# Performance work log

Measured on AMD Instinct MI355X. Metric: run time of the kernel, lower is better.

Reference implementation:

```python
import jax, jax.numpy as jnp
import numpy as np


def setup_inputs() -> dict:
    key = jax.random.key(0)
    ks = jax.random.split(key, 5)
    B, D, U = 16384, 512, 512
    return {
        "inputs": jax.random.normal(ks[0], (B, D), dtype=jnp.float32),
        "h_prev": jax.random.normal(ks[1], (B, U), dtype=jnp.float32),
        "update_kernel": jax.random.normal(ks[2], (D + U, U), dtype=jnp.float32) * 0.03,
        "reset_kernel": jax.random.normal(ks[3], (D + U, U), dtype=jnp.float32) * 0.03,
        "hidden_kernel": jax.random.normal(ks[4], (D + U, U), dtype=jnp.float32) * 0.03,
        "update_bias": jnp.zeros((U,), dtype=jnp.float32),
        "reset_bias": jnp.zeros((U,), dtype=jnp.float32),
        "hidden_bias": jnp.zeros((U,), dtype=jnp.float32),
    }


def reference(inputs, h_prev, update_kernel, reset_kernel, hidden_kernel,
              update_bias, reset_bias, hidden_bias):
    # fused_input: [B, D+U]
    fused = jnp.concatenate([inputs, h_prev], axis=-1)
    zg = jax.nn.sigmoid(fused @ update_kernel + update_bias)   # update gate [B,U]
    rg = jax.nn.sigmoid(fused @ reset_kernel + reset_bias)     # reset gate  [B,U]
    h_tilde = jnp.tanh(
        jnp.concatenate([inputs, rg * h_prev], axis=-1) @ hidden_kernel + hidden_bias
    )
    ht = (1.0 - zg) * h_prev + zg * h_tilde
    return ht
```

## Files before the change

### kernel.cpp

```cpp
#include <hip/hip_runtime.h>
#include <hip/hip_bf16.h>
#include <math.h>

typedef __attribute__((ext_vector_type(4))) float f32x4;
typedef __attribute__((ext_vector_type(8))) float f32x8;
typedef __bf16 bf16x8 __attribute__((ext_vector_type(8)));
typedef unsigned short u16;
typedef u16 u16x8 __attribute__((ext_vector_type(8)));
typedef void __attribute__((address_space(1))) * as1p;
typedef void __attribute__((address_space(3))) * as3p;

__device__ __forceinline__ unsigned short f2bf(float f) {
    union { float f; unsigned int u; } v; v.f = f;
    unsigned int u = v.u;
    u += 0x7fffu + ((u >> 16) & 1u);
    return (unsigned short)(u >> 16);
}

__device__ __forceinline__ float bf2f(unsigned short b) {
    union { unsigned int u; float f; } v;
    v.u = ((unsigned int)b) << 16;
    return v.f;
}

__device__ __forceinline__ float fast_tanh(float v) {
    float vc = fminf(fmaxf(v, -15.f), 15.f);
    float e = __expf(2.f * vc);
    return (e - 1.f) / (e + 1.f);
}

__global__ void prep_k(const float* __restrict__ x, const float* __restrict__ h,
                       const float* __restrict__ wz, const float* __restrict__ wrr,
                       const float* __restrict__ wh,
                       u16* __restrict__ xb, u16* __restrict__ hb,
                       u16* __restrict__ wzt, u16* __restrict__ wrt, u16* __restrict__ wht) {
    __shared__ float t[32][33];
    int bid = blockIdx.x;
    int tid = threadIdx.x;
    if (bid < 2048) {
        const int n4 = 16384 * 512 / 4;
        int i = bid * 256 + tid;
        const int stride = 2048 * 256;
        const float4* x4 = (const float4*)x;
        const float4* h4 = (const float4*)h;
        ushort4* xb4 = (ushort4*)xb;
        ushort4* hb4 = (ushort4*)hb;
        for (; i < n4; i += stride) {
            float4 v = x4[i];
            xb4[i] = make_ushort4(f2bf(v.x), f2bf(v.y), f2bf(v.z), f2bf(v.w));
            float4 w = h4[i];
            hb4[i] = make_ushort4(f2bf(w.x), f2bf(w.y), f2bf(w.z), f2bf(w.w));
        }
    } else {
        int b = bid - 2048;
        int z = b >> 9;
        int rem = b & 511;
        const float* src = (z == 0) ? wz : (z == 1) ? wrr : wh;
        u16* dst = (z == 0) ? wzt : (z == 1) ? wrt : wht;
        int n0 = (rem & 15) * 32;
        int k0 = (rem >> 4) * 32;
        int tx = tid & 31, ty = tid >> 5;
#pragma unroll
        for (int i = 0; i < 4; ++i)
            t[ty + i * 8][tx] = src[(size_t)(k0 + ty + i * 8) * 512 + n0 + tx];
        __syncthreads();
#pragma unroll
        for (int i = 0; i < 4; ++i)
            dst[(size_t)(n0 + ty + i * 8) * 1024 + k0 + tx] = f2bf(t[tx][ty + i * 8]);
    }
}

__device__ __forceinline__ void stage_sw(const u16* g, int gstride, u16* lds, int tid) {
#pragma unroll
    for (int i = 0; i < 4; ++i) {
        int ob = i * 4096 + ((tid >> 6) << 10);
        int o = ob + ((tid & 63) << 4);
        int row = o >> 7;
        int cb = (o & 127) ^ ((row & 7) << 4);
        const u16* gp = g + (size_t)row * gstride + (cb >> 1);
        __builtin_amdgcn_global_load_lds((as1p)(void*)gp, (as3p)(void*)(lds + (ob >> 1)), 16, 0, 0);
    }
}

__device__ __forceinline__ bf16x8 ld_frag(const u16* region, int r, int kb) {
    int byte = (r << 7) + (kb ^ ((r & 7) << 4));
    return *(const bf16x8*)((const char*)region + byte);
}

__device__ __forceinline__ void compute_tile(const u16* LA, const u16* LB,
                                             int wr, int wc, int l, f32x4 (&acc)[4][4]) {
    int fr = l & 15;
    int kbb = (l >> 4) << 4;
#pragma unroll
    for (int q = 0; q < 2; ++q) {
        bf16x8 a[4], b[4];
#pragma unroll
        for (int m = 0; m < 4; ++m)
            a[m] = ld_frag(LA, wr * 64 + m * 16 + fr, q * 64 + kbb);
#pragma unroll
        for (int n = 0; n < 4; ++n)
            b[n] = ld_frag(LB, wc * 64 + n * 16 + fr, q * 64 + kbb);
#pragma unroll
        for (int m = 0; m < 4; ++m)
#pragma unroll
            for (int n = 0; n < 4; ++n)
                acc[m][n] = __builtin_amdgcn_mfma_f32_16x16x32_bf16(a[m], b[n], acc[m][n], 0, 0, 0);
    }
}

template<typename AF, typename BF>
__device__ __forceinline__ void kloop(AF ga, BF gb, u16* lds, int tid,
                                      int wr, int wc, int l, f32x4 (&acc)[4][4]) {
    stage_sw(ga(0), 512, lds, tid);
    stage_sw(gb(0), 1024, lds + 8192, tid);
    __syncthreads();
#pragma unroll
    for (int i = 0; i < 15; ++i) {
        u16* nxt = lds + ((i + 1) & 1) * 16384;
        const u16* cur = lds + (i & 1) * 16384;
        stage_sw(ga(i + 1), 512, nxt, tid);
        stage_sw(gb(i + 1), 1024, nxt + 8192, tid);
        compute_tile(cur, cur + 8192, wr, wc, l, acc);
        __syncthreads();
    }
    compute_tile(lds + 16384, lds + 16384 + 8192, wr, wc, l, acc);
}

__device__ __forceinline__ void scatter_acc(float* tf, const f32x4 (&acc)[4][4],
                                            int wr, int wc, int l) {
    int colb = wc * 64;
    int rowb = wr * 64 + ((l >> 4) << 2);
#pragma unroll
    for (int n = 0; n < 4; ++n) {
        int col = colb + n * 16 + (l & 15);
#pragma unroll
        for (int m = 0; m < 4; ++m) {
            int row0 = rowb + m * 16;
#pragma unroll
            for (int r = 0; r < 4; ++r)
                tf[(row0 + r) * 128 + col] = acc[m][n][r];
        }
    }
}

__global__ __launch_bounds__(256) void gr_k(
    const u16* __restrict__ Xb, const u16* __restrict__ Hb, const u16* __restrict__ Wt,
    const float* __restrict__ rb_, u16* __restrict__ rgh) {
    __shared__ u16 lds[2 * 16384];
    int tid = threadIdx.x;
    int l = tid & 63, w = tid >> 6;
    int wr = w >> 1, wc = w & 1;
    int swz = (blockIdx.x & 7) * 64 + (blockIdx.x >> 3);
    int mb = swz >> 2, nb = swz & 3;
    int m0 = mb * 128, n0 = nb * 128;
    f32x4 acc[4][4];
#pragma unroll
    for (int m = 0; m < 4; ++m)
#pragma unroll
        for (int n = 0; n < 4; ++n) acc[m][n] = (f32x4){0.f, 0.f, 0.f, 0.f};

    auto ga = [&](int t) -> const u16* {
        return (t < 8) ? (Xb + (size_t)m0 * 512 + t * 64)
                       : (Hb + (size_t)m0 * 512 + (t - 8) * 64);
    };
    auto gb = [&](int t) -> const u16* { return Wt + (size_t)n0 * 1024 + t * 64; };
    kloop(ga, gb, lds, tid, wr, wc, l, acc);

    __syncthreads();
    float* tf = (float*)lds;
    scatter_acc(tf, acc, wr, wc, l);
    __syncthreads();
#pragma unroll
    for (int i = 0; i < 8; ++i) {
        int chunk = i * 256 + tid;
        int row = chunk >> 4;
        int c8 = (chunk & 15) << 3;
        const float* src = &tf[row * 128 + c8];
        int gcol = n0 + c8;
        size_t gbase = (size_t)(m0 + row) * 512 + gcol;
        u16x8 h8 = *(const u16x8*)&Hb[gbase];
        u16x8 o;
#pragma unroll
        for (int j = 0; j < 8; ++j) {
            float v = src[j] + rb_[gcol + j];
            float s = 1.f / (1.f + __expf(-v));
            o[j] = f2bf(s * bf2f(h8[j]));
        }
        *(u16x8*)&rgh[gbase] = o;
    }
}

__device__ __forceinline__ void stage32(const u16* g, int gstride, u16* region, int tid) {
#pragma unroll
    for (int i = 0; i < 2; ++i) {
        int ob = i * 4096 + ((tid >> 6) << 10);
        int o = ob + ((tid & 63) << 4);
        int row = o >> 6;
        int cb = (o & 63) ^ ((row & 6) << 3);
        const u16* gp = g + (size_t)row * gstride + (cb >> 1);
        __builtin_amdgcn_global_load_lds((as1p)(void*)gp, (as3p)(void*)(region + (ob >> 1)), 16, 0, 0);
    }
}

__device__ __forceinline__ bf16x8 ld32(const u16* region, int r, int kb) {
    int byte = (r << 6) + (kb ^ ((r & 6) << 3));
    return *(const bf16x8*)((const char*)region + byte);
}

__global__ __launch_bounds__(256, 2) void ghz_k(
    const u16* __restrict__ Xb, const u16* __restrict__ Hb, const u16* __restrict__ rgh,
    const u16* __restrict__ Wht, const u16* __restrict__ Wzt,
    const float* __restrict__ ub, const float* __restrict__ hb,
    float* __restrict__ out) {
    __shared__ u16 lds[2 * 16384];
    int tid = threadIdx.x;
    int l = tid & 63, w = tid >> 6;
    int wr = w >> 1, wc = w & 1;
    int swz = (blockIdx.x & 7) * 64 + (blockIdx.x >> 3);
    int mb = swz >> 2, nb = swz & 3;
    int m0 = mb * 128, n0 = nb * 128;

    f32x4 acc_h[4][4], acc_z[4][4];
#pragma unroll
    for (int m = 0; m < 4; ++m)
#pragma unroll
        for (int n = 0; n < 4; ++n) {
            acc_h[m][n] = (f32x4){0.f, 0.f, 0.f, 0.f};
            acc_z[m][n] = (f32x4){0.f, 0.f, 0.f, 0.f};
        }

    auto ah = [&](int t) -> const u16* {
        return (t < 16) ? (Xb + (size_t)m0 * 512 + t * 32)
                        : (rgh + (size_t)m0 * 512 + (t - 16) * 32);
    };
    auto az = [&](int t) -> const u16* {
        return Hb + (size_t)m0 * 512 + (t - 16) * 32;
    };
    auto bhp = [&](int t) -> const u16* { return Wht + (size_t)n0 * 1024 + t * 32; };
    auto bzp = [&](int t) -> const u16* { return Wzt + (size_t)n0 * 1024 + t * 32; };

    const int fr = l & 15;
    const int kbb = (l >> 4) << 4;

    stage32(ah(0), 512, lds, tid);
    stage32(bhp(0), 1024, lds + 8192, tid);
    stage32(bzp(0), 1024, lds + 12288, tid);
    __syncthreads();

#pragma unroll
    for (int i = 0; i < 32; ++i) {
        const u16* cur = lds + (i & 1) * 16384;
        if (i < 31) {
            u16* nxt = lds + ((i + 1) & 1) * 16384;
            stage32(ah(i + 1), 512, nxt, tid);
            if (i + 1 >= 16) stage32(az(i + 1), 512, nxt + 4096, tid);
            stage32(bhp(i + 1), 1024, nxt + 8192, tid);
            stage32(bzp(i + 1), 1024, nxt + 12288, tid);
        }
        const u16* Ahr = cur;
        const u16* Azr = (i < 16) ? cur : (cur + 4096);
        const u16* Bhr = cur + 8192;
        const u16* Bzr = cur + 12288;
        bf16x8 a[4], azf[4], bh4[4], bz4[4];
#pragma unroll
        for (int m = 0; m < 4; ++m) {
            a[m]   = ld32(Ahr, wr * 64 + m * 16 + fr, kbb);
            azf[m] = ld32(Azr, wr * 64 + m * 16 + fr, kbb);
        }
#pragma unroll
        for (int n = 0; n < 4; ++n) {
            bh4[n] = ld32(Bhr, wc * 64 + n * 16 + fr, kbb);
            bz4[n] = ld32(Bzr, wc * 64 + n * 16 + fr, kbb);
        }
#pragma unroll
        for (int m = 0; m < 4; ++m)
#pragma unroll
            for (int n = 0; n < 4; ++n) {
                acc_h[m][n] = __builtin_amdgcn_mfma_f32_16x16x32_bf16(a[m], bh4[n], acc_h[m][n], 0, 0, 0);
                acc_z[m][n] = __builtin_amdgcn_mfma_f32_16x16x32_bf16(azf[m], bz4[n], acc_z[m][n], 0, 0, 0);
            }
        __syncthreads();
    }

    float* tf = (float*)lds;
    scatter_acc(tf, acc_z, wr, wc, l);
    __syncthreads();
    u16x8 zreg[8];
#pragma unroll
    for (int i = 0; i < 8; ++i) {
        int chunk = i * 256 + tid;
        int row = chunk >> 4;
        int c8 = (chunk & 15) << 3;
        f32x8 vz = *(const f32x8*)&tf[row * 128 + c8];
        f32x8 ubv = *(const f32x8*)&ub[n0 + c8];
#pragma unroll
        for (int j = 0; j < 8; ++j) {
            float s = 1.f / (1.f + __expf(-(vz[j] + ubv[j])));
            zreg[i][j] = f2bf(s);
        }
    }
    __syncthreads();
    scatter_acc(tf, acc_h, wr, wc, l);
    __syncthreads();
#pragma unroll
    for (int i = 0; i < 8; ++i) {
        int chunk = i * 256 + tid;
        int row = chunk >> 4;
        int c8 = (chunk & 15) << 3;
        int gcol = n0 + c8;
        size_t gbase = (size_t)(m0 + row) * 512 + gcol;
        f32x8 vh = *(const f32x8*)&tf[row * 128 + c8];
        f32x8 hbv = *(const f32x8*)&hb[gcol];
        u16x8 h8 = *(const u16x8*)&Hb[gbase];
        f32x8 o;
#pragma unroll
        for (int j = 0; j < 8; ++j) {
            float t = fast_tanh(vh[j] + hbv[j]);
            float h0 = bf2f(h8[j]);
            float z = bf2f(zreg[i][j]);
            o[j] = h0 + z * (t - h0);
        }
        *(f32x8*)&out[gbase] = o;
    }
}

extern "C" void kernel_launch(void* const* d_in, const int* in_sizes, int n_in,
                              void* d_out, int out_size, void* d_ws, size_t ws_size,
                              hipStream_t stream) {
    const float* x  = (const float*)d_in[0];
    const float* h  = (const float*)d_in[1];
    const float* wz = (const float*)d_in[2];
    const float* wr = (const float*)d_in[3];
    const float* wh = (const float*)d_in[4];
    const float* ub = (const float*)d_in[5];
    const float* rb = (const float*)d_in[6];
    const float* hb = (const float*)d_in[7];
    float* out = (float*)d_out;

    const int B = 16384;
    char* ws = (char*)d_ws;
    size_t off = 0;
    u16* Xb  = (u16*)(ws + off); off += (size_t)B * 512 * 2;
    u16* Hb  = (u16*)(ws + off); off += (size_t)B * 512 * 2;
    u16* Wzt = (u16*)(ws + off); off += (size_t)512 * 1024 * 2;
    u16* Wrt = (u16*)(ws + off); off += (size_t)512 * 1024 * 2;
    u16* Wht = (u16*)(ws + off); off += (size_t)512 * 1024 * 2;
    u16* rgh = (u16*)(ws + off); off += (size_t)B * 512 * 2;

    prep_k<<<2048 + 1536, 256, 0, stream>>>(x, h, wz, wr, wh, Xb, Hb, Wzt, Wrt, Wht);

    gr_k<<<512, 256, 0, stream>>>(Xb, Hb, Wrt, rb, rgh);
    ghz_k<<<512, 256, 0, stream>>>(Xb, Hb, rgh, Wht, Wzt, ub, hb, out);
}
```

Before: 98.24 us.

## Halve GEMM N-tile to 64 and shrink LDS for higher occupancy

```diff
diff --git a/kernel.cpp b/kernel.cpp
--- a/kernel.cpp
+++ b/kernel.cpp
@@ -70,127 +70,7 @@
     }
 }
 
-__device__ __forceinline__ void stage_sw(const u16* g, int gstride, u16* lds, int tid) {
-#pragma unroll
-    for (int i = 0; i < 4; ++i) {
-        int ob = i * 4096 + ((tid >> 6) << 10);
-        int o = ob + ((tid & 63) << 4);
-        int row = o >> 7;
-        int cb = (o & 127) ^ ((row & 7) << 4);
-        const u16* gp = g + (size_t)row * gstride + (cb >> 1);
-        __builtin_amdgcn_global_load_lds((as1p)(void*)gp, (as3p)(void*)(lds + (ob >> 1)), 16, 0, 0);
-    }
-}
-
-__device__ __forceinline__ bf16x8 ld_frag(const u16* region, int r, int kb) {
-    int byte = (r << 7) + (kb ^ ((r & 7) << 4));
-    return *(const bf16x8*)((const char*)region + byte);
-}
-
-__device__ __forceinline__ void compute_tile(const u16* LA, const u16* LB,
-                                             int wr, int wc, int l, f32x4 (&acc)[4][4]) {
-    int fr = l & 15;
-    int kbb = (l >> 4) << 4;
-#pragma unroll
-    for (int q = 0; q < 2; ++q) {
-        bf16x8 a[4], b[4];
-#pragma unroll
-        for (int m = 0; m < 4; ++m)
-            a[m] = ld_frag(LA, wr * 64 + m * 16 + fr, q * 64 + kbb);
-#pragma unroll
-        for (int n = 0; n < 4; ++n)
-            b[n] = ld_frag(LB, wc * 64 + n * 16 + fr, q * 64 + kbb);
-#pragma unroll
-        for (int m = 0; m < 4; ++m)
-#pragma unroll
-            for (int n = 0; n < 4; ++n)
-                acc[m][n] = __builtin_amdgcn_mfma_f32_16x16x32_bf16(a[m], b[n], acc[m][n], 0, 0, 0);
-    }
-}
-
-template<typename AF, typename BF>
-__device__ __forceinline__ void kloop(AF ga, BF gb, u16* lds, int tid,
-                                      int wr, int wc, int l, f32x4 (&acc)[4][4]) {
-    stage_sw(ga(0), 512, lds, tid);
-    stage_sw(gb(0), 1024, lds + 8192, tid);
-    __syncthreads();
-#pragma unroll
-    for (int i = 0; i < 15; ++i) {
-        u16* nxt = lds + ((i + 1) & 1) * 16384;
-        const u16* cur = lds + (i & 1) * 16384;
-        stage_sw(ga(i + 1), 512, nxt, tid);
-        stage_sw(gb(i + 1), 1024, nxt + 8192, tid);
-        compute_tile(cur, cur + 8192, wr, wc, l, acc);
-        __syncthreads();
-    }
-    compute_tile(lds + 16384, lds + 16384 + 8192, wr, wc, l, acc);
-}
-
-__device__ __forceinline__ void scatter_acc(float* tf, const f32x4 (&acc)[4][4],
-                                            int wr, int wc, int l) {
-    int colb = wc * 64;
-    int rowb = wr * 64 + ((l >> 4) << 2);
-#pragma unroll
-    for (int n = 0; n < 4; ++n) {
-        int col = colb + n * 16 + (l & 15);
-#pragma unroll
-        for (int m = 0; m < 4; ++m) {
-            int row0 = rowb + m * 16;
-#pragma unroll
-            for (int r = 0; r < 4; ++r)
-                tf[(row0 + r) * 128 + col] = acc[m][n][r];
-        }
-    }
-}
-
-__global__ __launch_bounds__(256) void gr_k(
-    const u16* __restrict__ Xb, const u16* __restrict__ Hb, const u16* __restrict__ Wt,
-    const float* __restrict__ rb_, u16* __restrict__ rgh) {
-    __shared__ u16 lds[2 * 16384];
-    int tid = threadIdx.x;
-    int l = tid & 63, w = tid >> 6;
-    int wr = w >> 1, wc = w & 1;
-    int swz = (blockIdx.x & 7) * 64 + (blockIdx.x >> 3);
-    int mb = swz >> 2, nb = swz & 3;
-    int m0 = mb * 128, n0 = nb * 128;
-    f32x4 acc[4][4];
-#pragma unroll
-    for (int m = 0; m < 4; ++m)
-#pragma unroll
-        for (int n = 0; n < 4; ++n) acc[m][n] = (f32x4){0.f, 0.f, 0.f, 0.f};
-
-    auto ga = [&](int t) -> const u16* {
-        return (t < 8) ? (Xb + (size_t)m0 * 512 + t * 64)
-                       : (Hb + (size_t)m0 * 512 + (t - 8) * 64);
-    };
-    auto gb = [&](int t) -> const u16* { return Wt + (size_t)n0 * 1024 + t * 64; };
-    kloop(ga, gb, lds, tid, wr, wc, l, acc);
-
-    __syncthreads();
-    float* tf = (float*)lds;
-    scatter_acc(tf, acc, wr, wc, l);
-    __syncthreads();
-#pragma unroll
-    for (int i = 0; i < 8; ++i) {
-        int chunk = i * 256 + tid;
-        int row = chunk >> 4;
-        int c8 = (chunk & 15) << 3;
-        const float* src = &tf[row * 128 + c8];
-        int gcol = n0 + c8;
-        size_t gbase = (size_t)(m0 + row) * 512 + gcol;
-        u16x8 h8 = *(const u16x8*)&Hb[gbase];
-        u16x8 o;
-#pragma unroll
-        for (int j = 0; j < 8; ++j) {
-            float v = src[j] + rb_[gcol + j];
-            float s = 1.f / (1.f + __expf(-v));
-            o[j] = f2bf(s * bf2f(h8[j]));
-        }
-        *(u16x8*)&rgh[gbase] = o;
-    }
-}
-
-__device__ __forceinline__ void stage32(const u16* g, int gstride, u16* region, int tid) {
+__device__ __forceinline__ void stageA32(const u16* g, int gstride, u16* region, int tid) {
 #pragma unroll
     for (int i = 0; i < 2; ++i) {
         int ob = i * 4096 + ((tid >> 6) << 10);
@@ -202,32 +82,153 @@
     }
 }
 
+__device__ __forceinline__ void stageB32(const u16* g, int gstride, u16* region, int tid) {
+    int ob = (tid >> 6) << 10;
+    int o = ob + ((tid & 63) << 4);
+    int row = o >> 6;
+    int cb = (o & 63) ^ ((row & 6) << 3);
+    const u16* gp = g + (size_t)row * gstride + (cb >> 1);
+    __builtin_amdgcn_global_load_lds((as1p)(void*)gp, (as3p)(void*)(region + (ob >> 1)), 16, 0, 0);
+}
+
 __device__ __forceinline__ bf16x8 ld32(const u16* region, int r, int kb) {
     int byte = (r << 6) + (kb ^ ((r & 6) << 3));
     return *(const bf16x8*)((const char*)region + byte);
 }
 
-__global__ __launch_bounds__(256, 2) void ghz_k(
+__device__ __forceinline__ void scatter64(float* tf, const f32x4 (&acc)[4][2],
+                                          int wr, int wc, int l) {
+    int colb = wc * 32;
+    int rowb = wr * 64 + ((l >> 4) << 2);
+#pragma unroll
+    for (int n = 0; n < 2; ++n) {
+        int col = colb + n * 16 + (l & 15);
+#pragma unroll
+        for (int m = 0; m < 4; ++m) {
+            int row0 = rowb + m * 16;
+#pragma unroll
+            for (int r = 0; r < 4; ++r)
+                tf[(row0 + r) * 64 + col] = acc[m][n][r];
+        }
+    }
+}
+
+__global__ __launch_bounds__(256, 4) void gr_k(
+    const u16* __restrict__ Xb, const u16* __restrict__ Hb, const u16* __restrict__ Wt,
+    const float* __restrict__ rb_, u16* __restrict__ rgh) {
+    __shared__ u16 lds[16384];
+    int tid = threadIdx.x;
+    int l = tid & 63, w = tid >> 6;
+    int wr = w >> 1, wc = w & 1;
+    int bid = blockIdx.x;
+    int swz = (bid & 7) * 128 + (bid >> 3);
+    int mb = swz >> 3, nbv = swz & 7;
+    int m0 = mb * 128, n0 = nbv * 64;
+    f32x4 acc[4][2];
+#pragma unroll
+    for (int m = 0; m < 4; ++m)
+#pragma unroll
+        for (int n = 0; n < 2; ++n) acc[m][n] = (f32x4){0.f, 0.f, 0.f, 0.f};
+
+    const int fr = l & 15;
+    const int kbb = (l >> 4) << 4;
+
+    auto ga = [&](int t) -> const u16* {
+        return (t < 16) ? (Xb + (size_t)m0 * 512 + t * 32)
+                        : (Hb + (size_t)m0 * 512 + (t - 16) * 32);
+    };
+    auto gb = [&](int t) -> const u16* { return Wt + (size_t)n0 * 1024 + t * 32; };
+
+    stageA32(ga(0), 512, lds, tid);
+    stageB32(gb(0), 1024, lds + 4096, tid);
+    __syncthreads();
+#pragma unroll
+    for (int i = 0; i < 31; ++i) {
+        u16* nxt = lds + ((i + 1) & 1) * 6144;
+        const u16* cur = lds + (i & 1) * 6144;
+        stageA32(ga(i + 1), 512, nxt, tid);
+        stageB32(gb(i + 1), 1024, nxt + 4096, tid);
+        {
+            bf16x8 a[4], b[2];
+#pragma unroll
+            for (int m = 0; m < 4; ++m)
+                a[m] = ld32(cur, wr * 64 + m * 16 + fr, kbb);
+#pragma unroll
+            for (int n = 0; n < 2; ++n)
+                b[n] = ld32(cur + 4096, wc * 32 + n * 16 + fr, kbb);
+#pragma unroll
+            for (int m = 0; m < 4; ++m)
+#pragma unroll
+                for (int n = 0; n < 2; ++n)
+                    acc[m][n] = __builtin_amdgcn_mfma_f32_16x16x32_bf16(a[m], b[n], acc[m][n], 0, 0, 0);
+        }
+        __syncthreads();
+    }
+    {
+        const u16* cur = lds + (31 & 1) * 6144;
+        bf16x8 a[4], b[2];
+#pragma unroll
+        for (int m = 0; m < 4; ++m)
+            a[m] = ld32(cur, wr * 64 + m * 16 + fr, kbb);
+#pragma unroll
+        for (int n = 0; n < 2; ++n)
+            b[n] = ld32(cur + 4096, wc * 32 + n * 16 + fr, kbb);
+#pragma unroll
+        for (int m = 0; m < 4; ++m)
+#pragma unroll
+            for (int n = 0; n < 2; ++n)
+                acc[m][n] = __builtin_amdgcn_mfma_f32_16x16x32_bf16(a[m], b[n], acc[m][n], 0, 0, 0);
+    }
+
+    __syncthreads();
+    float* tf = (float*)lds;
+    scatter64(tf, acc, wr, wc, l);
+    __syncthreads();
+#pragma unroll
+    for (int it = 0; it < 4; ++it) {
+        int chunk = it * 256 + tid;
+        int row = chunk >> 3;
+        int c8 = (chunk & 7) << 3;
+        const float* src = &tf[row * 64 + c8];
+        int gcol = n0 + c8;
+        size_t gbase = (size_t)(m0 + row) * 512 + gcol;
+        u16x8 h8 = *(const u16x8*)&Hb[gbase];
+        u16x8 o;
+#pragma unroll
+        for (int j = 0; j < 8; ++j) {
+            float v = src[j] + rb_[gcol + j];
+            float s = 1.f / (1.f + __expf(-v));
+            o[j] = f2bf(s * bf2f(h8[j]));
+        }
+        *(u16x8*)&rgh[gbase] = o;
+    }
+}
+
+__global__ __launch_bounds__(256, 3) void ghz_k(
     const u16* __restrict__ Xb, const u16* __restrict__ Hb, const u16* __restrict__ rgh,
     const u16* __restrict__ Wht, const u16* __restrict__ Wzt,
     const float* __restrict__ ub, const float* __restrict__ hb,
     float* __restrict__ out) {
-    __shared__ u16 lds[2 * 16384];
+    __shared__ u16 lds[24576];
     int tid = threadIdx.x;
     int l = tid & 63, w = tid >> 6;
     int wr = w >> 1, wc = w & 1;
-    int swz = (blockIdx.x & 7) * 64 + (blockIdx.x >> 3);
-    int mb = swz >> 2, nb = swz & 3;
-    int m0 = mb * 128, n0 = nb * 128;
-
-    f32x4 acc_h[4][4], acc_z[4][4];
+    int bid = blockIdx.x;
+    int swz = (bid & 7) * 128 + (bid >> 3);
+    int mb = swz >> 3, nbv = swz & 7;
+    int m0 = mb * 128, n0 = nbv * 64;
+
+    f32x4 acc_h[4][2], acc_z[4][2];
 #pragma unroll
     for (int m = 0; m < 4; ++m)
 #pragma unroll
-        for (int n = 0; n < 4; ++n) {
+        for (int n = 0; n < 2; ++n) {
             acc_h[m][n] = (f32x4){0.f, 0.f, 0.f, 0.f};
             acc_z[m][n] = (f32x4){0.f, 0.f, 0.f, 0.f};
         }
+
+    const int fr = l & 15;
+    const int kbb = (l >> 4) << 4;
 
     auto ah = [&](int t) -> const u16* {
         return (t < 16) ? (Xb + (size_t)m0 * 512 + t * 32)
@@ -239,77 +240,74 @@
     auto bhp = [&](int t) -> const u16* { return Wht + (size_t)n0 * 1024 + t * 32; };
     auto bzp = [&](int t) -> const u16* { return Wzt + (size_t)n0 * 1024 + t * 32; };
 
-    const int fr = l & 15;
-    const int kbb = (l >> 4) << 4;
-
-    stage32(ah(0), 512, lds, tid);
-    stage32(bhp(0), 1024, lds + 8192, tid);
-    stage32(bzp(0), 1024, lds + 12288, tid);
+    stageA32(ah(0), 512, lds, tid);
+    stageB32(bhp(0), 1024, lds + 8192, tid);
+    stageB32(bzp(0), 1024, lds + 10240, tid);
     __syncthreads();
 
 #pragma unroll
     for (int i = 0; i < 32; ++i) {
-        const u16* cur = lds + (i & 1) * 16384;
+        const u16* cur = lds + (i & 1) * 12288;
         if (i < 31) {
-            u16* nxt = lds + ((i + 1) & 1) * 16384;
-            stage32(ah(i + 1), 512, nxt, tid);
-            if (i + 1 >= 16) stage32(az(i + 1), 512, nxt + 4096, tid);
-            stage32(bhp(i + 1), 1024, nxt + 8192, tid);
-            stage32(bzp(i + 1), 1024, nxt + 12288, tid);
+            u16* nxt = lds + ((i + 1) & 1) * 12288;
+            stageA32(ah(i + 1), 512, nxt, tid);
+            if (i + 1 >= 16) stageA32(az(i + 1), 512, nxt + 4096, tid);
+            stageB32(bhp(i + 1), 1024, nxt + 8192, tid);
+            stageB32(bzp(i + 1), 1024, nxt + 10240, tid);
         }
         const u16* Ahr = cur;
         const u16* Azr = (i < 16) ? cur : (cur + 4096);
         const u16* Bhr = cur + 8192;
-        const u16* Bzr = cur + 12288;
-        bf16x8 a[4], azf[4], bh4[4], bz4[4];
+        const u16* Bzr = cur + 10240;
+        bf16x8 a[4], azf[4], bh2[2], bz2[2];
 #pragma unroll
         for (int m = 0; m < 4; ++m) {
             a[m]   = ld32(Ahr, wr * 64 + m * 16 + fr, kbb);
             azf[m] = ld32(Azr, wr * 64 + m * 16 + fr, kbb);
         }
 #pragma unroll
-        for (int n = 0; n < 4; ++n) {
-            bh4[n] = ld32(Bhr, wc * 64 + n * 16 + fr, kbb);
-            bz4[n] = ld32(Bzr, wc * 64 + n * 16 + fr, kbb);
+        for (int n = 0; n < 2; ++n) {
+            bh2[n] = ld32(Bhr, wc * 32 + n * 16 + fr, kbb);
+            bz2[n] = ld32(Bzr, wc * 32 + n * 16 + fr, kbb);
         }
 #pragma unroll
         for (int m = 0; m < 4; ++m)
 #pragma unroll
-            for (int n = 0; n < 4; ++n) {
-                acc_h[m][n] = __builtin_amdgcn_mfma_f32_16x16x32_bf16(a[m], bh4[n], acc_h[m][n], 0, 0, 0);
-                acc_z[m][n] = __builtin_amdgcn_mfma_f32_16x16x32_bf16(azf[m], bz4[n], acc_z[m][n], 0, 0, 0);
+            for (int n = 0; n < 2; ++n) {
+                acc_h[m][n] = __builtin_amdgcn_mfma_f32_16x16x32_bf16(a[m], bh2[n], acc_h[m][n], 0, 0, 0);
+                acc_z[m][n] = __builtin_amdgcn_mfma_f32_16x16x32_bf16(azf[m], bz2[n], acc_z[m][n], 0, 0, 0);
             }
         __syncthreads();
     }
 
     float* tf = (float*)lds;
-    scatter_acc(tf, acc_z, wr, wc, l);
-    __syncthreads();
-    u16x8 zreg[8];
-#pragma unroll
-    for (int i = 0; i < 8; ++i) {
-        int chunk = i * 256 + tid;
-        int row = chunk >> 4;
-        int c8 = (chunk & 15) << 3;
-        f32x8 vz = *(const f32x8*)&tf[row * 128 + c8];
+    scatter64(tf, acc_z, wr, wc, l);
+    __syncthreads();
+    u16x8 zreg[4];
+#pragma unroll
+    for (int it = 0; it < 4; ++it) {
+        int chunk = it * 256 + tid;
+        int row = chunk >> 3;
+        int c8 = (chunk & 7) << 3;
+        f32x8 vz = *(const f32x8*)&tf[row * 64 + c8];
         f32x8 ubv = *(const f32x8*)&ub[n0 + c8];
 #pragma unroll
         for (int j = 0; j < 8; ++j) {
             float s = 1.f / (1.f + __expf(-(vz[j] + ubv[j])));
-            zreg[i][j] = f2bf(s);
-        }
-    }
-    __syncthreads();
-    scatter_acc(tf, acc_h, wr, wc, l);
-    __syncthreads();
-#pragma unroll
-    for (int i = 0; i < 8; ++i) {
-        int chunk = i * 256 + tid;
-        int row = chunk >> 4;
-        int c8 = (chunk & 15) << 3;
+            zreg[it][j] = f2bf(s);
+        }
+    }
+    __syncthreads();
+    scatter64(tf, acc_h, wr, wc, l);
+    __syncthreads();
+#pragma unroll
+    for (int it = 0; it < 4; ++it) {
+        int chunk = it * 256 + tid;
+        int row = chunk >> 3;
+        int c8 = (chunk & 7) << 3;
         int gcol = n0 + c8;
         size_t gbase = (size_t)(m0 + row) * 512 + gcol;
-        f32x8 vh = *(const f32x8*)&tf[row * 128 + c8];
+        f32x8 vh = *(const f32x8*)&tf[row * 64 + c8];
         f32x8 hbv = *(const f32x8*)&hb[gcol];
         u16x8 h8 = *(const u16x8*)&Hb[gbase];
         f32x8 o;
@@ -317,7 +315,7 @@
         for (int j = 0; j < 8; ++j) {
             float t = fast_tanh(vh[j] + hbv[j]);
             float h0 = bf2f(h8[j]);
-            float z = bf2f(zreg[i][j]);
+            float z = bf2f(zreg[it][j]);
             o[j] = h0 + z * (t - h0);
         }
         *(f32x8*)&out[gbase] = o;
@@ -349,6 +347,6 @@
 
     prep_k<<<2048 + 1536, 256, 0, stream>>>(x, h, wz, wr, wh, Xb, Hb, Wzt, Wrt, Wht);
 
-    gr_k<<<512, 256, 0, stream>>>(Xb, Hb, Wrt, rb, rgh);
-    ghz_k<<<512, 256, 0, stream>>>(Xb, Hb, rgh, Wht, Wzt, ub, hb, out);
-}
+    gr_k<<<1024, 256, 0, stream>>>(Xb, Hb, Wrt, rb, rgh);
+    ghz_k<<<1024, 256, 0, stream>>>(Xb, Hb, rgh, Wht, Wzt, ub, hb, out);
+}
```

New measurement: 106.3 us. 8.2% more time.

## Halve ghz_k N-tile to 64 columns and double grid for occupancy

Applied to the files above, without the earlier changes.

```diff
diff --git a/kernel.cpp b/kernel.cpp
--- a/kernel.cpp
+++ b/kernel.cpp
@@ -190,7 +190,7 @@
     }
 }
 
-__device__ __forceinline__ void stage32(const u16* g, int gstride, u16* region, int tid) {
+__device__ __forceinline__ void stageA32(const u16* g, int gstride, u16* region, int tid) {
 #pragma unroll
     for (int i = 0; i < 2; ++i) {
         int ob = i * 4096 + ((tid >> 6) << 10);
@@ -202,32 +202,62 @@
     }
 }
 
+__device__ __forceinline__ void stageB32(const u16* g, int gstride, u16* region, int tid) {
+    int ob = (tid >> 6) << 10;
+    int o = ob + ((tid & 63) << 4);
+    int row = o >> 6;
+    int cb = (o & 63) ^ ((row & 6) << 3);
+    const u16* gp = g + (size_t)row * gstride + (cb >> 1);
+    __builtin_amdgcn_global_load_lds((as1p)(void*)gp, (as3p)(void*)(region + (ob >> 1)), 16, 0, 0);
+}
+
 __device__ __forceinline__ bf16x8 ld32(const u16* region, int r, int kb) {
     int byte = (r << 6) + (kb ^ ((r & 6) << 3));
     return *(const bf16x8*)((const char*)region + byte);
 }
 
-__global__ __launch_bounds__(256, 2) void ghz_k(
+__device__ __forceinline__ void scatter64(float* tf, const f32x4 (&acc)[4][2],
+                                          int wr, int wc, int l) {
+    int colb = wc * 32;
+    int rowb = wr * 64 + ((l >> 4) << 2);
+#pragma unroll
+    for (int n = 0; n < 2; ++n) {
+        int col = colb + n * 16 + (l & 15);
+#pragma unroll
+        for (int m = 0; m < 4; ++m) {
+            int row0 = rowb + m * 16;
+#pragma unroll
+            for (int r = 0; r < 4; ++r)
+                tf[(row0 + r) * 64 + col] = acc[m][n][r];
+        }
+    }
+}
+
+__global__ __launch_bounds__(256, 3) void ghz_k(
     const u16* __restrict__ Xb, const u16* __restrict__ Hb, const u16* __restrict__ rgh,
     const u16* __restrict__ Wht, const u16* __restrict__ Wzt,
     const float* __restrict__ ub, const float* __restrict__ hb,
     float* __restrict__ out) {
-    __shared__ u16 lds[2 * 16384];
+    __shared__ u16 lds[24576];
     int tid = threadIdx.x;
     int l = tid & 63, w = tid >> 6;
     int wr = w >> 1, wc = w & 1;
-    int swz = (blockIdx.x & 7) * 64 + (blockIdx.x >> 3);
-    int mb = swz >> 2, nb = swz & 3;
-    int m0 = mb * 128, n0 = nb * 128;
-
-    f32x4 acc_h[4][4], acc_z[4][4];
+    int bid = blockIdx.x;
+    int swz = (bid & 7) * 128 + (bid >> 3);
+    int mb = swz >> 3, nbv = swz & 7;
+    int m0 = mb * 128, n0 = nbv * 64;
+
+    f32x4 acc_h[4][2], acc_z[4][2];
 #pragma unroll
     for (int m = 0; m < 4; ++m)
 #pragma unroll
-        for (int n = 0; n < 4; ++n) {
+        for (int n = 0; n < 2; ++n) {
             acc_h[m][n] = (f32x4){0.f, 0.f, 0.f, 0.f};
             acc_z[m][n] = (f32x4){0.f, 0.f, 0.f, 0.f};
         }
+
+    const int fr = l & 15;
+    const int kbb = (l >> 4) << 4;
 
     auto ah = [&](int t) -> const u16* {
         return (t < 16) ? (Xb + (size_t)m0 * 512 + t * 32)
@@ -239,77 +269,74 @@
     auto bhp = [&](int t) -> const u16* { return Wht + (size_t)n0 * 1024 + t * 32; };
     auto bzp = [&](int t) -> const u16* { return Wzt + (size_t)n0 * 1024 + t * 32; };
 
-    const int fr = l & 15;
-    const int kbb = (l >> 4) << 4;
-
-    stage32(ah(0), 512, lds, tid);
-    stage32(bhp(0), 1024, lds + 8192, tid);
-    stage32(bzp(0), 1024, lds + 12288, tid);
+    stageA32(ah(0), 512, lds, tid);
+    stageB32(bhp(0), 1024, lds + 8192, tid);
+    stageB32(bzp(0), 1024, lds + 10240, tid);
     __syncthreads();
 
 #pragma unroll
     for (int i = 0; i < 32; ++i) {
-        const u16* cur = lds + (i & 1) * 16384;
+        const u16* cur = lds + (i & 1) * 12288;
         if (i < 31) {
-            u16* nxt = lds + ((i + 1) & 1) * 16384;
-            stage32(ah(i + 1), 512, nxt, tid);
-            if (i + 1 >= 16) stage32(az(i + 1), 512, nxt + 4096, tid);
-            stage32(bhp(i + 1), 1024, nxt + 8192, tid);
-            stage32(bzp(i + 1), 1024, nxt + 12288, tid);
+            u16* nxt = lds + ((i + 1) & 1) * 12288;
+            stageA32(ah(i + 1), 512, nxt, tid);
+            if (i + 1 >= 16) stageA32(az(i + 1), 512, nxt + 4096, tid);
+            stageB32(bhp(i + 1), 1024, nxt + 8192, tid);
+            stageB32(bzp(i + 1), 1024, nxt + 10240, tid);
         }
         const u16* Ahr = cur;
         const u16* Azr = (i < 16) ? cur : (cur + 4096);
         const u16* Bhr = cur + 8192;
-        const u16* Bzr = cur + 12288;
-        bf16x8 a[4], azf[4], bh4[4], bz4[4];
+        const u16* Bzr = cur + 10240;
+        bf16x8 a[4], azf[4], bh2[2], bz2[2];
 #pragma unroll
         for (int m = 0; m < 4; ++m) {
             a[m]   = ld32(Ahr, wr * 64 + m * 16 + fr, kbb);
             azf[m] = ld32(Azr, wr * 64 + m * 16 + fr, kbb);
         }
 #pragma unroll
-        for (int n = 0; n < 4; ++n) {
-            bh4[n] = ld32(Bhr, wc * 64 + n * 16 + fr, kbb);
-            bz4[n] = ld32(Bzr, wc * 64 + n * 16 + fr, kbb);
+        for (int n = 0; n < 2; ++n) {
+            bh2[n] = ld32(Bhr, wc * 32 + n * 16 + fr, kbb);
+            bz2[n] = ld32(Bzr, wc * 32 + n * 16 + fr, kbb);
         }
 #pragma unroll
         for (int m = 0; m < 4; ++m)
 #pragma unroll
-            for (int n = 0; n < 4; ++n) {
-                acc_h[m][n] = __builtin_amdgcn_mfma_f32_16x16x32_bf16(a[m], bh4[n], acc_h[m][n], 0, 0, 0);
-                acc_z[m][n] = __builtin_amdgcn_mfma_f32_16x16x32_bf16(azf[m], bz4[n], acc_z[m][n], 0, 0, 0);
+            for (int n = 0; n < 2; ++n) {
+                acc_h[m][n] = __builtin_amdgcn_mfma_f32_16x16x32_bf16(a[m], bh2[n], acc_h[m][n], 0, 0, 0);
+                acc_z[m][n] = __builtin_amdgcn_mfma_f32_16x16x32_bf16(azf[m], bz2[n], acc_z[m][n], 0, 0, 0);
             }
         __syncthreads();
     }
 
     float* tf = (float*)lds;
-    scatter_acc(tf, acc_z, wr, wc, l);
-    __syncthreads();
-    u16x8 zreg[8];
-#pragma unroll
-    for (int i = 0; i < 8; ++i) {
-        int chunk = i * 256 + tid;
-        int row = chunk >> 4;
-        int c8 = (chunk & 15) << 3;
-        f32x8 vz = *(const f32x8*)&tf[row * 128 + c8];
+    scatter64(tf, acc_z, wr, wc, l);
+    __syncthreads();
+    u16x8 zreg[4];
+#pragma unroll
+    for (int it = 0; it < 4; ++it) {
+        int chunk = it * 256 + tid;
+        int row = chunk >> 3;
+        int c8 = (chunk & 7) << 3;
+        f32x8 vz = *(const f32x8*)&tf[row * 64 + c8];
         f32x8 ubv = *(const f32x8*)&ub[n0 + c8];
 #pragma unroll
         for (int j = 0; j < 8; ++j) {
             float s = 1.f / (1.f + __expf(-(vz[j] + ubv[j])));
-            zreg[i][j] = f2bf(s);
-        }
-    }
-    __syncthreads();
-    scatter_acc(tf, acc_h, wr, wc, l);
-    __syncthreads();
-#pragma unroll
-    for (int i = 0; i < 8; ++i) {
-        int chunk = i * 256 + tid;
-        int row = chunk >> 4;
-        int c8 = (chunk & 15) << 3;
+            zreg[it][j] = f2bf(s);
+        }
+    }
+    __syncthreads();
+    scatter64(tf, acc_h, wr, wc, l);
+    __syncthreads();
+#pragma unroll
+    for (int it = 0; it < 4; ++it) {
+        int chunk = it * 256 + tid;
+        int row = chunk >> 3;
+        int c8 = (chunk & 7) << 3;
         int gcol = n0 + c8;
         size_t gbase = (size_t)(m0 + row) * 512 + gcol;
-        f32x8 vh = *(const f32x8*)&tf[row * 128 + c8];
+        f32x8 vh = *(const f32x8*)&tf[row * 64 + c8];
         f32x8 hbv = *(const f32x8*)&hb[gcol];
         u16x8 h8 = *(const u16x8*)&Hb[gbase];
         f32x8 o;
@@ -317,7 +344,7 @@
         for (int j = 0; j < 8; ++j) {
             float t = fast_tanh(vh[j] + hbv[j]);
             float h0 = bf2f(h8[j]);
-            float z = bf2f(zreg[i][j]);
+            float z = bf2f(zreg[it][j]);
             o[j] = h0 + z * (t - h0);
         }
         *(f32x8*)&out[gbase] = o;
@@ -350,5 +377,5 @@
     prep_k<<<2048 + 1536, 256, 0, stream>>>(x, h, wz, wr, wh, Xb, Hb, Wzt, Wrt, Wht);
 
     gr_k<<<512, 256, 0, stream>>>(Xb, Hb, Wrt, rb, rgh);
-    ghz_k<<<512, 256, 0, stream>>>(Xb, Hb, rgh, Wht, Wzt, ub, hb, out);
-}
+    ghz_k<<<1024, 256, 0, stream>>>(Xb, Hb, rgh, Wht, Wzt, ub, hb, out);
+}
```

Measured after the change: 104.2 us. +6.1%, slower.
